# Optimization experiments

Hardware: AMD Instinct MI355X
Metric: run time of the kernel (lower is better)

The kernel has to match this reference:

```python
import jax, jax.numpy as jnp
import numpy as np
import math

N_HEADS = 4
IN_DIM = 1024
DIM_HEAD = IN_DIM // N_HEADS


def setup_inputs() -> dict:
    key = jax.random.key(0)
    ks = jax.random.split(key, 5)
    x = jax.random.normal(ks[0], (8, 2048, IN_DIM), dtype=jnp.float32)
    std = 0.02
    W_Q = jax.random.normal(ks[1], (N_HEADS, IN_DIM, DIM_HEAD), dtype=jnp.float32) * std
    W_K = jax.random.normal(ks[2], (N_HEADS, IN_DIM, DIM_HEAD), dtype=jnp.float32) * std
    W_V = jax.random.normal(ks[3], (N_HEADS, IN_DIM, DIM_HEAD), dtype=jnp.float32) * std
    W_O = jax.random.normal(ks[4], (N_HEADS, DIM_HEAD, IN_DIM), dtype=jnp.float32) * std
    b_Q = jnp.zeros((N_HEADS, DIM_HEAD), dtype=jnp.float32)
    b_K = jnp.zeros((N_HEADS, DIM_HEAD), dtype=jnp.float32)
    b_V = jnp.zeros((N_HEADS, DIM_HEAD), dtype=jnp.float32)
    b_O = jnp.zeros((IN_DIM,), dtype=jnp.float32)
    return {"normalized_resid_pre": x, "W_Q": W_Q, "b_Q": b_Q, "W_K": W_K,
            "b_K": b_K, "W_V": W_V, "b_V": b_V, "W_O": W_O, "b_O": b_O}


def reference(normalized_resid_pre, W_Q, b_Q, W_K, b_K, W_V, b_V, W_O, b_O):
    x = normalized_resid_pre  # [n, s, d_model]
    # projections: [n, s, h, dh]
    q = jnp.einsum('nsd,hde->nshe', x, W_Q) + b_Q
    k = jnp.einsum('nsd,hde->nshe', x, W_K) + b_K
    v = jnp.einsum('nsd,hde->nshe', x, W_V) + b_V
    scale = 1.0 / math.sqrt(DIM_HEAD)
    scores = jnp.einsum('nqhe,nkhe->nhqk', q, k) * scale  # [n, h, q, k]
    pattern = jax.nn.softmax(scores, axis=-1)
    z = jnp.einsum('nhqk,nkhe->nqhe', pattern, v)  # [n, q, h, dh]
    out = jnp.einsum('nqhe,hed->nqd', z, W_O) + b_O  # [n, q, d_model]
    return out
```

## Files before the change

### kernel.cpp

```cpp
#include <hip/hip_runtime.h>

typedef __attribute__((ext_vector_type(8))) short short8;
typedef __attribute__((ext_vector_type(4))) float floatx4;
typedef __attribute__((ext_vector_type(16))) float floatx16;
typedef __attribute__((ext_vector_type(4))) unsigned short ushort4v;
typedef __attribute__((ext_vector_type(2))) unsigned int uint2v;
typedef unsigned short u16;

__device__ __forceinline__ u16 f2bf(float f) {
  unsigned u = __float_as_uint(f);
  u += 0x7fffu + ((u >> 16) & 1u);
  return (u16)(u >> 16);
}

__device__ __forceinline__ void gl_lds16(const void* g, void* l) {
  __builtin_amdgcn_global_load_lds((const __attribute__((address_space(1))) void*)g,
                                   (__attribute__((address_space(3))) void*)l, 16, 0, 0);
}

__device__ __forceinline__ float bpermf(float v, int srclane) {
  return __int_as_float(__builtin_amdgcn_ds_bpermute(srclane << 2, __float_as_int(v)));
}

#define BARRIER() do { asm volatile("" ::: "memory"); __builtin_amdgcn_s_barrier(); asm volatile("" ::: "memory"); } while (0)


__global__ void k_cvt_x(const float* __restrict__ x, u16* __restrict__ o, long n) {
  long i = ((long)blockIdx.x * blockDim.x + threadIdx.x) * 8;
  long stride = (long)gridDim.x * blockDim.x * 8;
  for (; i < n; i += stride) {
    float4 a = *(const float4*)(x + i);
    float4 b = *(const float4*)(x + i + 4);
    ushort4v r0 = { f2bf(a.x), f2bf(a.y), f2bf(a.z), f2bf(a.w) };
    ushort4v r1 = { f2bf(b.x), f2bf(b.y), f2bf(b.z), f2bf(b.w) };
    *(ushort4v*)(o + i) = r0;
    *(ushort4v*)(o + i + 4) = r1;
  }
}

__global__ __launch_bounds__(256) void k_cvt_w(
    const float* __restrict__ WQ, const float* __restrict__ WK,
    const float* __restrict__ WV, const float* __restrict__ WO,
    u16* __restrict__ wqkv, u16* __restrict__ wo) {
  __shared__ float tile[64][65];
  const int bid = blockIdx.x;
  const float* src;
  u16* dst;
  int C, R, r0, c0;
  if (bid < 768) {
    int th = bid >> 6;
    int tid6 = bid & 63;
    int t = th >> 2, h = th & 3;
    src = ((t == 0) ? WQ : (t == 1) ? WK : WV) + h * 1024 * 256;
    dst = wqkv + (size_t)(t * 1024 + h * 256) * 1024;
    R = 1024; C = 256;
    r0 = (tid6 & 15) * 64;
    c0 = (tid6 >> 4) * 64;
  } else {
    int tid6 = bid - 768;
    src = WO; dst = wo;
    R = 1024; C = 1024;
    r0 = (tid6 & 15) * 64;
    c0 = (tid6 >> 4) * 64;
  }
  const int tx = threadIdx.x & 15, ty = threadIdx.x >> 4;
#pragma unroll
  for (int i = 0; i < 4; ++i) {
    int r = ty + 16 * i;
    float4 v = *(const float4*)(src + (long)(r0 + r) * C + c0 + tx * 4);
    tile[r][tx * 4 + 0] = v.x;
    tile[r][tx * 4 + 1] = v.y;
    tile[r][tx * 4 + 2] = v.z;
    tile[r][tx * 4 + 3] = v.w;
  }
  __syncthreads();
#pragma unroll
  for (int i = 0; i < 4; ++i) {
    int c = ty + 16 * i;
    ushort4v o = { f2bf(tile[tx * 4 + 0][c]), f2bf(tile[tx * 4 + 1][c]),
                   f2bf(tile[tx * 4 + 2][c]), f2bf(tile[tx * 4 + 3][c]) };
    *(ushort4v*)(dst + (long)(c0 + c) * R + r0 + tx * 4) = o;
  }
}

template<int EPI>
__global__ __launch_bounds__(512, 2) void k_gemm8(
    const u16* __restrict__ A, const u16* __restrict__ Bt,
    u16* __restrict__ Qo, u16* __restrict__ Ko, u16* __restrict__ Vt,
    const float* __restrict__ bQ, const float* __restrict__ bK, const float* __restrict__ bV,
    float* __restrict__ out, const float* __restrict__ bO, int gridNx) {
  extern __shared__ char lds[];
  const int tid = threadIdx.x, lane = tid & 63, w = tid >> 6;
  const int wm = w >> 2, wn = w & 3;
  const int cI = lane & 15, rI = lane >> 4;
  const int nwg = gridDim.x;
  const int bid = blockIdx.x;
  const int swz = (bid & 7) * (nwg >> 3) + (bid >> 3);
  const int by = swz / gridNx, bx = swz % gridNx;
  const long am0 = (long)by * 256, bn0 = (long)bx * 256;

  int so_ds[2], so_src[2];
#pragma unroll
  for (int jj = 0; jj < 2; ++jj) {
    int o = jj * 8192 + tid * 16;
    int row = o >> 7;
    so_ds[jj] = o;
    so_src[jj] = row * 1024 + ((((o >> 4) & 7) ^ (row & 7)) << 3);
  }
  const u16* gAlo = A + am0 * 1024;
  const u16* gAhi = gAlo + 128 * 1024;
  const u16* gBlo = Bt + bn0 * 1024;
  const u16* gBhi = gBlo + 128 * 1024;

#define STG(gp, kt, ldsbyte) do { \
    gl_lds16((gp) + (kt) * 64 + so_src[0], lds + (ldsbyte) + so_ds[0]); \
    gl_lds16((gp) + (kt) * 64 + so_src[1], lds + (ldsbyte) + so_ds[1]); \
  } while (0)

  floatx4 acc[8][4] = {};

  STG(gAlo, 0, 0);
  STG(gBlo, 0, 65536);
  STG(gAhi, 0, 16384);
  STG(gBhi, 0, 81920);
  STG(gAlo, 1, 32768);
  STG(gBlo, 1, 98304);
  asm volatile("s_waitcnt vmcnt(4)" ::: "memory");
  BARRIER();

#define PHASE(AB, BB, MH, NH, STAGE_STMT, VMSTMT) do { \
    short8 af[4][2], bf[2][2]; \
    _Pragma("unroll") \
    for (int mi2 = 0; mi2 < 4; ++mi2) { \
      int row = wm * 64 + mi2 * 16 + cI; \
      const char* rp = lds + (AB) + (MH) * 16384 + row * 128; \
      int sw = row & 7; \
      _Pragma("unroll") \
      for (int kk = 0; kk < 2; ++kk) \
        af[mi2][kk] = *(const short8*)(rp + (((kk * 4 + rI) ^ sw) << 4)); \
    } \
    _Pragma("unroll") \
    for (int ni2 = 0; ni2 < 2; ++ni2) { \
      int row = wn * 32 + ni2 * 16 + cI; \
      const char* rp = lds + (BB) + (NH) * 16384 + row * 128; \
      int sw = row & 7; \
      _Pragma("unroll") \
      for (int kk = 0; kk < 2; ++kk) \
        bf[ni2][kk] = *(const short8*)(rp + (((kk * 4 + rI) ^ sw) << 4)); \
    } \
    STAGE_STMT; \
    VMSTMT; \
    BARRIER(); \
    __builtin_amdgcn_s_setprio(1); \
    _Pragma("unroll") \
    for (int mi2 = 0; mi2 < 4; ++mi2) \
      _Pragma("unroll") \
      for (int ni2 = 0; ni2 < 2; ++ni2) \
        _Pragma("unroll") \
        for (int kk = 0; kk < 2; ++kk) \
          acc[(MH) * 4 + mi2][(NH) * 2 + ni2] = __builtin_amdgcn_mfma_f32_16x16x32_bf16( \
              af[mi2][kk], bf[ni2][kk], acc[(MH) * 4 + mi2][(NH) * 2 + ni2], 0, 0, 0); \
    __builtin_amdgcn_s_setprio(0); \
    BARRIER(); \
  } while (0)

  for (int it = 0; it < 8; ++it) {
    const int u = 2 * it;
    const bool s2 = (u + 2 < 16), s3 = (u + 3 < 16);
    PHASE(0, 65536, 0, 0, STG(gAhi, u + 1, 49152), );
    PHASE(0, 65536, 0, 1, STG(gBhi, u + 1, 114688), );
    PHASE(0, 65536, 1, 0, if (s2) STG(gAlo, u + 2, 0), );
    PHASE(0, 65536, 1, 1, if (s2) STG(gBlo, u + 2, 65536),
          if (s2) { asm volatile("s_waitcnt vmcnt(4)" ::: "memory"); }
          else    { asm volatile("s_waitcnt vmcnt(0)" ::: "memory"); });
    PHASE(32768, 98304, 0, 0, if (s2) STG(gAhi, u + 2, 16384), );
    PHASE(32768, 98304, 0, 1, if (s2) STG(gBhi, u + 2, 81920), );
    PHASE(32768, 98304, 1, 0, if (s3) STG(gAlo, u + 3, 32768), );
    PHASE(32768, 98304, 1, 1, if (s3) STG(gBlo, u + 3, 98304),
          asm volatile("s_waitcnt vmcnt(4)" ::: "memory"));
  }

  if (EPI == 0) {
    const int t = (int)(bn0 >> 10);
    const int h = (int)(bn0 >> 8) & 3;
    const float* bias = (t == 0) ? bQ : (t == 1) ? bK : bV;
    const float sc = (t == 0) ? 0.0625f * 1.44269504088896f : 1.0f;
#pragma unroll
    for (int MH = 0; MH < 2; ++MH)
#pragma unroll
    for (int mi = 0; mi < 4; ++mi) {
      int m = (int)am0 + MH * 128 + wm * 64 + mi * 16 + rI * 4;
      int b = m >> 11, s = m & 2047;
#pragma unroll
      for (int NH = 0; NH < 2; ++NH)
#pragma unroll
      for (int ni = 0; ni < 2; ++ni) {
        int e = NH * 128 + wn * 32 + ni * 16 + cI;
        float bb = bias[h * 256 + e];
        floatx4 c = acc[MH * 4 + mi][NH * 2 + ni];
        if (t < 2) {
          u16* dst = (t == 0) ? Qo : Ko;
          long base = ((long)(b * 4 + h) * 2048 + s) * 256 + e;
          dst[base]       = f2bf((c[0] + bb) * sc);
          dst[base + 256] = f2bf((c[1] + bb) * sc);
          dst[base + 512] = f2bf((c[2] + bb) * sc);
          dst[base + 768] = f2bf((c[3] + bb) * sc);
        } else {
          long base = ((long)(b * 4 + h) * 256 + e) * 2048 + s;
          ushort4v v = { f2bf(c[0] + bb), f2bf(c[1] + bb), f2bf(c[2] + bb), f2bf(c[3] + bb) };
          *(ushort4v*)(Vt + base) = v;
        }
      }
    }
  } else {
#pragma unroll
    for (int MH = 0; MH < 2; ++MH)
#pragma unroll
    for (int mi = 0; mi < 4; ++mi) {
      int m = (int)am0 + MH * 128 + wm * 64 + mi * 16 + rI * 4;
#pragma unroll
      for (int NH = 0; NH < 2; ++NH)
#pragma unroll
      for (int ni = 0; ni < 2; ++ni) {
        int n = (int)bn0 + NH * 128 + wn * 32 + ni * 16 + cI;
        float bb = bO[n];
        floatx4 c = acc[MH * 4 + mi][NH * 2 + ni];
        out[(long)m * 1024 + n]       = c[0] + bb;
        out[(long)(m + 1) * 1024 + n] = c[1] + bb;
        out[(long)(m + 2) * 1024 + n] = c[2] + bb;
        out[(long)(m + 3) * 1024 + n] = c[3] + bb;
      }
    }
  }
#undef PHASE
#undef STG
}

__global__ __launch_bounds__(256, 2) void k_attn(
    const u16* __restrict__ Q, const u16* __restrict__ K,
    const u16* __restrict__ Vt, u16* __restrict__ Z) {
  extern __shared__ u16 smem[];
  u16* sK = smem;
  u16* sV = smem + 16384;
  const int tid = threadIdx.x, lane = tid & 63, w = tid >> 6;
  const int q = lane & 31, hi = lane >> 5;
  const int role = (blockIdx.x & 7) * 64 + (blockIdx.x >> 3);
  const int bh = role >> 4, qt = role & 15;
  const long base = (long)bh * 2048 * 256;
  const int q0 = qt * 128 + w * 32;

  int off_ds[4], ksrc[4], vsrc[4];
#pragma unroll
  for (int j = 0; j < 4; ++j) {
    int o = j * 4096 + tid * 16;
    off_ds[j] = o;
    int krow = o >> 9, kch = (o >> 4) & 31;
    ksrc[j] = krow * 256 + ((kch ^ (krow & 7)) << 3);
    int e = o >> 6, cr = (o >> 4) & 3;
    vsrc[j] = e * 2048 + ((cr ^ ((e >> 1) & 3)) << 3);
  }
  const u16* Kg0 = K + base;
  const u16* Vg  = Vt + base;

  short8 qf[16];
#pragma unroll
  for (int ec = 0; ec < 16; ++ec)
    qf[ec] = *(const short8*)(Q + base + (long)(q0 + q) * 256 + ec * 16 + hi * 8);

#define STAGE_K(kt_, buf_) do { \
    const u16* Kg_ = Kg0 + (kt_) * 8192; \
    u16* dK_ = sK + (buf_) * 8192; \
    _Pragma("unroll") \
    for (int j = 0; j < 4; ++j) gl_lds16(Kg_ + ksrc[j], (char*)dK_ + off_ds[j]); \
  } while (0)
#define STAGE_V(kt_, buf_) do { \
    const u16* Vg_ = Vg + (kt_) * 32; \
    u16* dV_ = sV + (buf_) * 8192; \
    _Pragma("unroll") \
    for (int j = 0; j < 4; ++j) gl_lds16(Vg_ + vsrc[j], (char*)dV_ + off_ds[j]); \
  } while (0)

  STAGE_K(0, 0);

  floatx16 z[8] = {};
  float m_run = -1e30f, l = 0.f;
  const int ksw = q & 7, vsw = (q >> 1) & 3;
  short8 pa0 = {}, pa1 = {};

  __syncthreads();

  for (int t = 0; t < 64; ++t) {
    const int cb = t & 1;
    if (t < 63) STAGE_K(t + 1, cb ^ 1);
    STAGE_V(t, cb);
    const char* pK = (const char*)(sK + cb * 8192);
    const char* pV = (const char*)(sV + (cb ^ 1) * 8192);

    floatx16 s = {};
    __builtin_amdgcn_s_setprio(1);
    if (t > 0) {
#pragma unroll
      for (int u = 0; u < 8; ++u) {
        short8 kf0 = *(const short8*)(pK + (q << 9) + ((((4 * u) | hi) ^ ksw) << 4));
        s = __builtin_amdgcn_mfma_f32_32x32x16_bf16(kf0, qf[2 * u], s, 0, 0, 0);
        short8 vf0 = *(const short8*)(pV + ((u * 32 + q) << 6) + (((hi ^ vsw) & 3) << 4));
        z[u] = __builtin_amdgcn_mfma_f32_32x32x16_bf16(pa0, vf0, z[u], 0, 0, 0);
        short8 kf1 = *(const short8*)(pK + (q << 9) + ((((4 * u + 2) | hi) ^ ksw) << 4));
        s = __builtin_amdgcn_mfma_f32_32x32x16_bf16(kf1, qf[2 * u + 1], s, 0, 0, 0);
        short8 vf1 = *(const short8*)(pV + ((u * 32 + q) << 6) + ((((2 | hi) ^ vsw) & 3) << 4));
        z[u] = __builtin_amdgcn_mfma_f32_32x32x16_bf16(pa1, vf1, z[u], 0, 0, 0);
      }
    } else {
#pragma unroll
      for (int ec = 0; ec < 16; ++ec) {
        short8 kf = *(const short8*)(pK + (q << 9) + ((((2 * ec) | hi) ^ ksw) << 4));
        s = __builtin_amdgcn_mfma_f32_32x32x16_bf16(kf, qf[ec], s, 0, 0, 0);
      }
    }
    __builtin_amdgcn_s_setprio(0);

    float m0 = fmaxf(s[0], s[1]),  m1 = fmaxf(s[2], s[3]);
    float m2 = fmaxf(s[4], s[5]),  m3 = fmaxf(s[6], s[7]);
    float m4 = fmaxf(s[8], s[9]),  m5 = fmaxf(s[10], s[11]);
    float m6 = fmaxf(s[12], s[13]), m7 = fmaxf(s[14], s[15]);
    m0 = fmaxf(m0, m1); m2 = fmaxf(m2, m3); m4 = fmaxf(m4, m5); m6 = fmaxf(m6, m7);
    m0 = fmaxf(m0, m2); m4 = fmaxf(m4, m6);
    float pm = fmaxf(m0, m4);
    {
      uint2v sw = __builtin_amdgcn_permlane32_swap(__float_as_uint(pm), __float_as_uint(pm), false, false);
      pm = fmaxf(__uint_as_float(sw[0]), __uint_as_float(sw[1]));
    }

    if (!__all(pm <= m_run + 8.f)) {
      float mn = fmaxf(m_run, pm);
      float esc = exp2f(m_run - mn);
      l *= esc;
      m_run = mn;
      float escv[16];
#pragma unroll
      for (int r = 0; r < 16; ++r)
        escv[r] = bpermf(esc, ((r & 3) + 8 * (r >> 2) + 4 * hi) + 32 * hi);
#pragma unroll
      for (int et = 0; et < 8; ++et)
#pragma unroll
        for (int r = 0; r < 16; ++r) z[et][r] *= escv[r];
    }

    float p[16], rs = 0.f;
#pragma unroll
    for (int r = 0; r < 16; ++r) { p[r] = exp2f(s[r] - m_run); rs += p[r]; }
    {
      uint2v sw = __builtin_amdgcn_permlane32_swap(__float_as_uint(rs), __float_as_uint(rs), false, false);
      l += __uint_as_float(sw[0]) + __uint_as_float(sw[1]);
    }

    unsigned w0, w1, w2, w3, w4, w5, w6, w7;
    asm("v_cvt_pk_bf16_f32 %0, %1, %2" : "=v"(w0) : "v"(p[0]), "v"(p[1]));
    asm("v_cvt_pk_bf16_f32 %0, %1, %2" : "=v"(w1) : "v"(p[2]), "v"(p[3]));
    asm("v_cvt_pk_bf16_f32 %0, %1, %2" : "=v"(w2) : "v"(p[4]), "v"(p[5]));
    asm("v_cvt_pk_bf16_f32 %0, %1, %2" : "=v"(w3) : "v"(p[6]), "v"(p[7]));
    asm("v_cvt_pk_bf16_f32 %0, %1, %2" : "=v"(w4) : "v"(p[8]), "v"(p[9]));
    asm("v_cvt_pk_bf16_f32 %0, %1, %2" : "=v"(w5) : "v"(p[10]), "v"(p[11]));
    asm("v_cvt_pk_bf16_f32 %0, %1, %2" : "=v"(w6) : "v"(p[12]), "v"(p[13]));
    asm("v_cvt_pk_bf16_f32 %0, %1, %2" : "=v"(w7) : "v"(p[14]), "v"(p[15]));
    uint2v e02 = __builtin_amdgcn_permlane32_swap(w0, w2, false, false);
    uint2v e13 = __builtin_amdgcn_permlane32_swap(w1, w3, false, false);
    uint2v e46 = __builtin_amdgcn_permlane32_swap(w4, w6, false, false);
    uint2v e57 = __builtin_amdgcn_permlane32_swap(w5, w7, false, false);
    int4 t0i = { (int)e02[0], (int)e13[0], (int)e02[1], (int)e13[1] };
    int4 t1i = { (int)e46[0], (int)e57[0], (int)e46[1], (int)e57[1] };
    pa0 = *(short8*)&t0i;
    pa1 = *(short8*)&t1i;

    __syncthreads();
  }

  {
    const char* pV = (const char*)(sV + 8192);
#pragma unroll
    for (int u = 0; u < 8; ++u) {
      short8 vf0 = *(const short8*)(pV + ((u * 32 + q) << 6) + (((hi ^ vsw) & 3) << 4));
      z[u] = __builtin_amdgcn_mfma_f32_32x32x16_bf16(pa0, vf0, z[u], 0, 0, 0);
      short8 vf1 = *(const short8*)(pV + ((u * 32 + q) << 6) + ((((2 | hi) ^ vsw) & 3) << 4));
      z[u] = __builtin_amdgcn_mfma_f32_32x32x16_bf16(pa1, vf1, z[u], 0, 0, 0);
    }
  }

  float linv = 1.f / l;
  float invv[16];
#pragma unroll
  for (int r = 0; r < 16; ++r)
    invv[r] = bpermf(linv, ((r & 3) + 8 * (r >> 2) + 4 * hi) + 32 * hi);

  const int b = bh >> 2, hh = bh & 3;
  const long zb = (long)b * 2048 * 1024 + hh * 256;
#pragma unroll
  for (int r = 0; r < 16; ++r) {
    const int qr = (r & 3) + 8 * (r >> 2) + 4 * hi;
    long rb = zb + (long)(q0 + qr) * 1024;
#pragma unroll
    for (int et = 0; et < 8; ++et)
      Z[rb + et * 32 + q] = f2bf(z[et][r] * invv[r]);
  }
#undef STAGE_K
#undef STAGE_V
}


extern "C" void kernel_launch(void* const* d_in, const int* in_sizes, int n_in,
                              void* d_out, int out_size, void* d_ws, size_t ws_size,
                              hipStream_t stream) {
  const float* x  = (const float*)d_in[0];
  const float* WQ = (const float*)d_in[1];
  const float* bQ = (const float*)d_in[2];
  const float* WK = (const float*)d_in[3];
  const float* bK = (const float*)d_in[4];
  const float* WV = (const float*)d_in[5];
  const float* bV = (const float*)d_in[6];
  const float* WO = (const float*)d_in[7];
  const float* bO = (const float*)d_in[8];
  float* out = (float*)d_out;

  char* p = (char*)d_ws;
  u16* xb   = (u16*)p; p += (size_t)16384 * 1024 * 2;
  u16* wqkv = (u16*)p; p += (size_t)3072 * 1024 * 2;
  u16* wo   = (u16*)p; p += (size_t)1024 * 1024 * 2;
  u16* Qb   = (u16*)p; p += (size_t)32 * 2048 * 256 * 2;
  u16* Kb   = (u16*)p; p += (size_t)32 * 2048 * 256 * 2;
  u16* Vtb  = (u16*)p; p += (size_t)32 * 256 * 2048 * 2;
  u16* Zb   = xb;

  const int attn_lds = 65536;
  (void)hipFuncSetAttribute((const void*)k_attn,
                            hipFuncAttributeMaxDynamicSharedMemorySize, attn_lds);
  const int gemm_lds = 131072;
  (void)hipFuncSetAttribute((const void*)k_gemm8<0>,
                            hipFuncAttributeMaxDynamicSharedMemorySize, gemm_lds);
  (void)hipFuncSetAttribute((const void*)k_gemm8<1>,
                            hipFuncAttributeMaxDynamicSharedMemorySize, gemm_lds);

  k_cvt_x<<<dim3(4096), dim3(256), 0, stream>>>(x, xb, (long)16384 * 1024);
  k_cvt_w<<<dim3(1024), dim3(256), 0, stream>>>(WQ, WK, WV, WO, wqkv, wo);
  k_gemm8<0><<<dim3(768), dim3(512), gemm_lds, stream>>>(xb, wqkv, Qb, Kb, Vtb, bQ, bK, bV,
                                                         (float*)nullptr, (const float*)nullptr, 12);
  k_attn<<<dim3(512), dim3(256), attn_lds, stream>>>(Qb, Kb, Vtb, Zb);
  k_gemm8<1><<<dim3(256), dim3(512), gemm_lds, stream>>>(Zb, wo,
                                                         (u16*)nullptr, (u16*)nullptr, (u16*)nullptr,
                                                         (const float*)nullptr, (const float*)nullptr, (const float*)nullptr,
                                                         out, bO, 4);
}
```

Before: 360.0 us.

## Pre-tile K and V in projection epilogue to match MFMA fragment order

The projection epilogue now writes K and V into a blocked layout where each 32-key tile is contiguous and ordered exactly as the attention kernel's MFMA fragment loads consume it. The attention kernel then stages K/V tiles with fully contiguous 16-byte global-to-LDS copies and reads fragments at simple constant offsets, dropping the XOR swizzle and per-thread source address tables. This aims for coalesced global loads and less address arithmetic. The trade-offs are scattered 2-byte stores for K in the epilogue, and LDS reads that rely on the layout alone, without a swizzle, to avoid bank conflicts.

```diff
diff --git a/kernel.cpp b/kernel.cpp
--- a/kernel.cpp
+++ b/kernel.cpp
@@ -198,17 +198,24 @@
         int e = NH * 128 + wn * 32 + ni * 16 + cI;
         float bb = bias[h * 256 + e];
         floatx4 c = acc[MH * 4 + mi][NH * 2 + ni];
-        if (t < 2) {
-          u16* dst = (t == 0) ? Qo : Ko;
+        if (t == 0) {
           long base = ((long)(b * 4 + h) * 2048 + s) * 256 + e;
-          dst[base]       = f2bf((c[0] + bb) * sc);
-          dst[base + 256] = f2bf((c[1] + bb) * sc);
-          dst[base + 512] = f2bf((c[2] + bb) * sc);
-          dst[base + 768] = f2bf((c[3] + bb) * sc);
+          Qo[base]       = f2bf((c[0] + bb) * sc);
+          Qo[base + 256] = f2bf((c[1] + bb) * sc);
+          Qo[base + 512] = f2bf((c[2] + bb) * sc);
+          Qo[base + 768] = f2bf((c[3] + bb) * sc);
+        } else if (t == 1) {
+          long kb = ((long)(b * 4 + h) << 19) + ((long)(s >> 5) << 13) +
+                    ((e >> 3) << 8) + ((s & 31) << 3) + (e & 7);
+          Ko[kb]      = f2bf(c[0] + bb);
+          Ko[kb + 8]  = f2bf(c[1] + bb);
+          Ko[kb + 16] = f2bf(c[2] + bb);
+          Ko[kb + 24] = f2bf(c[3] + bb);
         } else {
-          long base = ((long)(b * 4 + h) * 256 + e) * 2048 + s;
+          long vb = ((long)(b * 4 + h) << 19) + ((long)(s >> 5) << 13) +
+                    (((s >> 3) & 3) << 11) + ((long)e << 3) + (s & 7);
           ushort4v v = { f2bf(c[0] + bb), f2bf(c[1] + bb), f2bf(c[2] + bb), f2bf(c[3] + bb) };
-          *(ushort4v*)(Vt + base) = v;
+          *(ushort4v*)(Vt + vb) = v;
         }
       }
     }
@@ -240,8 +247,8 @@
     const u16* __restrict__ Q, const u16* __restrict__ K,
     const u16* __restrict__ Vt, u16* __restrict__ Z) {
   extern __shared__ u16 smem[];
-  u16* sK = smem;
-  u16* sV = smem + 16384;
+  char* sKc = (char*)smem;
+  char* sVc = (char*)smem + 32768;
   const int tid = threadIdx.x, lane = tid & 63, w = tid >> 6;
   const int q = lane & 31, hi = lane >> 5;
   const int role = (blockIdx.x & 7) * 64 + (blockIdx.x >> 3);
@@ -249,18 +256,10 @@
   const long base = (long)bh * 2048 * 256;
   const int q0 = qt * 128 + w * 32;
 
-  int off_ds[4], ksrc[4], vsrc[4];
-#pragma unroll
-  for (int j = 0; j < 4; ++j) {
-    int o = j * 4096 + tid * 16;
-    off_ds[j] = o;
-    int krow = o >> 9, kch = (o >> 4) & 31;
-    ksrc[j] = krow * 256 + ((kch ^ (krow & 7)) << 3);
-    int e = o >> 6, cr = (o >> 4) & 3;
-    vsrc[j] = e * 2048 + ((cr ^ ((e >> 1) & 3)) << 3);
-  }
   const u16* Kg0 = K + base;
-  const u16* Vg  = Vt + base;
+  const u16* Vg0 = Vt + base;
+  const int stq = tid * 8;
+  const int dtq = tid * 16;
 
   short8 qf[16];
 #pragma unroll
@@ -268,23 +267,24 @@
     qf[ec] = *(const short8*)(Q + base + (long)(q0 + q) * 256 + ec * 16 + hi * 8);
 
 #define STAGE_K(kt_, buf_) do { \
-    const u16* Kg_ = Kg0 + (kt_) * 8192; \
-    u16* dK_ = sK + (buf_) * 8192; \
+    const u16* g_ = Kg0 + (kt_) * 8192 + stq; \
+    char* d_ = sKc + (buf_) * 16384 + dtq; \
     _Pragma("unroll") \
-    for (int j = 0; j < 4; ++j) gl_lds16(Kg_ + ksrc[j], (char*)dK_ + off_ds[j]); \
+    for (int j = 0; j < 4; ++j) gl_lds16(g_ + j * 2048, d_ + j * 4096); \
   } while (0)
 #define STAGE_V(kt_, buf_) do { \
-    const u16* Vg_ = Vg + (kt_) * 32; \
-    u16* dV_ = sV + (buf_) * 8192; \
+    const u16* g_ = Vg0 + (kt_) * 8192 + stq; \
+    char* d_ = sVc + (buf_) * 16384 + dtq; \
     _Pragma("unroll") \
-    for (int j = 0; j < 4; ++j) gl_lds16(Vg_ + vsrc[j], (char*)dV_ + off_ds[j]); \
+    for (int j = 0; j < 4; ++j) gl_lds16(g_ + j * 2048, d_ + j * 4096); \
   } while (0)
 
   STAGE_K(0, 0);
 
   floatx16 z[8] = {};
   float m_run = -1e30f, l = 0.f;
-  const int ksw = q & 7, vsw = (q >> 1) & 3;
+  const int kb = hi * 512 + q * 16;
+  const int vb = hi * 4096 + q * 16;
   short8 pa0 = {}, pa1 = {};
 
   __syncthreads();
@@ -293,27 +293,27 @@
     const int cb = t & 1;
     if (t < 63) STAGE_K(t + 1, cb ^ 1);
     STAGE_V(t, cb);
-    const char* pK = (const char*)(sK + cb * 8192);
-    const char* pV = (const char*)(sV + (cb ^ 1) * 8192);
+    const char* pK = sKc + cb * 16384 + kb;
+    const char* pV = sVc + (cb ^ 1) * 16384 + vb;
 
     floatx16 s = {};
     __builtin_amdgcn_s_setprio(1);
     if (t > 0) {
 #pragma unroll
       for (int u = 0; u < 8; ++u) {
-        short8 kf0 = *(const short8*)(pK + (q << 9) + ((((4 * u) | hi) ^ ksw) << 4));
+        short8 kf0 = *(const short8*)(pK + (2 * u) * 1024);
         s = __builtin_amdgcn_mfma_f32_32x32x16_bf16(kf0, qf[2 * u], s, 0, 0, 0);
-        short8 vf0 = *(const short8*)(pV + ((u * 32 + q) << 6) + (((hi ^ vsw) & 3) << 4));
+        short8 vf0 = *(const short8*)(pV + u * 512);
         z[u] = __builtin_amdgcn_mfma_f32_32x32x16_bf16(pa0, vf0, z[u], 0, 0, 0);
-        short8 kf1 = *(const short8*)(pK + (q << 9) + ((((4 * u + 2) | hi) ^ ksw) << 4));
+        short8 kf1 = *(const short8*)(pK + (2 * u + 1) * 1024);
         s = __builtin_amdgcn_mfma_f32_32x32x16_bf16(kf1, qf[2 * u + 1], s, 0, 0, 0);
-        short8 vf1 = *(const short8*)(pV + ((u * 32 + q) << 6) + ((((2 | hi) ^ vsw) & 3) << 4));
+        short8 vf1 = *(const short8*)(pV + 8192 + u * 512);
         z[u] = __builtin_amdgcn_mfma_f32_32x32x16_bf16(pa1, vf1, z[u], 0, 0, 0);
       }
     } else {
 #pragma unroll
       for (int ec = 0; ec < 16; ++ec) {
-        short8 kf = *(const short8*)(pK + (q << 9) + ((((2 * ec) | hi) ^ ksw) << 4));
+        short8 kf = *(const short8*)(pK + ec * 1024);
         s = __builtin_amdgcn_mfma_f32_32x32x16_bf16(kf, qf[ec], s, 0, 0, 0);
       }
     }
@@ -376,12 +376,12 @@
   }
 
   {
-    const char* pV = (const char*)(sV + 8192);
+    const char* pV = sVc + 16384 + vb;
 #pragma unroll
     for (int u = 0; u < 8; ++u) {
-      short8 vf0 = *(const short8*)(pV + ((u * 32 + q) << 6) + (((hi ^ vsw) & 3) << 4));
+      short8 vf0 = *(const short8*)(pV + u * 512);
       z[u] = __builtin_amdgcn_mfma_f32_32x32x16_bf16(pa0, vf0, z[u], 0, 0, 0);
-      short8 vf1 = *(const short8*)(pV + ((u * 32 + q) << 6) + ((((2 | hi) ^ vsw) & 3) << 4));
+      short8 vf1 = *(const short8*)(pV + 8192 + u * 512);
       z[u] = __builtin_amdgcn_mfma_f32_32x32x16_bf16(pa1, vf1, z[u], 0, 0, 0);
     }
   }
```

Result: faster. 325.3 us (-9.6%).
